# Kernel optimization log

Hardware: AMD Instinct MI355X
Metric: run time of the kernel (lower is better)

## Reference

```python
import jax, jax.numpy as jnp
import numpy as np

B, R, C, D = 8, 64, 16, 128  # batch, num_rows(taxa), patch_num, embed_dim


def _linear_init(key, fan_in, fan_out):
    lim = 1.0 / np.sqrt(fan_in)
    kw, kb = jax.random.split(key)
    W = jax.random.uniform(kw, (fan_in, fan_out), jnp.float32, -lim, lim)
    b = jax.random.uniform(kb, (fan_out,), jnp.float32, -lim, lim)
    return W, b


def setup_inputs() -> dict:
    key = jax.random.key(0)
    ks = jax.random.split(key, 8)
    row_np, col_np = np.triu_indices(R, k=1)  # n = R*(R-1)/2 = 2016 pairs
    hW, hb = _linear_init(ks[1], D, D)
    gW, gb = _linear_init(ks[2], D, D)
    qW, qb = _linear_init(ks[3], D, D)
    kW, kb = _linear_init(ks[4], D, D)
    s1W, s1b = _linear_init(ks[5], D, D)
    s2W, s2b = _linear_init(ks[6], D, 1)
    return {
        "batch_input": jax.random.normal(ks[0], (B, R, C, D), jnp.float32),
        "seq_mask": jnp.ones((B, 1, C), jnp.float32),
        "row": jnp.asarray(row_np, jnp.int32),
        "col": jnp.asarray(col_np, jnp.int32),
        "hW": hW, "hb": hb, "gW": gW, "gb": gb,
        "qW": qW, "qb": qb, "kW": kW, "kb": kb,
        "s1W": s1W, "s1b": s1b, "s2W": s2W, "s2b": s2b,
    }


def reference(batch_input, seq_mask, row, col,
              hW, hb, gW, gb, qW, qb, kW, kb, s1W, s1b, s2W, s2b):
    b, r, c, d = batch_input.shape
    n = row.shape[0]
    # pairwise gather: x_i, x_j -> [b, n, c, d]
    x_i = batch_input[:, row]
    x_j = batch_input[:, col]
    # sigmoid gate fusion of the pair
    h = (x_i - x_j) @ hW + hb
    z = jax.nn.sigmoid(h)
    x = z * x_i + (1.0 - z) * x_j
    # masked global attention over the batch_input 'memory' (r > 2 branch)
    q = x @ qW + qb                    # [b, n, c, d]
    k = batch_input @ kW + kb          # [b, r, c, d]
    scale = 1.0 / np.sqrt(d * c).astype(np.float32)
    alpha = jnp.einsum('bncd,brcd->bnr', q, k) * scale
    # -inf at (pair n, rows row[n] and col[n]); equivalent to += -inf on finite scores
    neg_mask = (jnp.zeros((n, r), bool)
                .at[jnp.arange(n), row].set(True)
                .at[jnp.arange(n), col].set(True))
    alpha = jnp.where(neg_mask[None], -jnp.inf, alpha)
    alpha = jax.nn.softmax(alpha, axis=-1)
    x_glob = jnp.einsum('bnr,brcd->bncd', alpha, batch_input)
    g = x_glob @ gW + gb
    w = jax.nn.sigmoid(g)
    x = (1.0 - w) * x + w * x_glob
    # s_out: Linear -> GELU(exact) -> Linear(d,1), then mask and reduce over c
    s = jax.nn.gelu(x @ s1W + s1b, approximate=False) @ s2W + s2b  # [b, n, c, 1]
    scores = s[..., 0] * seq_mask       # seq_mask [b,1,c] broadcasts over n
    return scores.sum(-1)               # [b, n]
```

## Files before the change

kernel.cpp:

```cpp
#include <hip/hip_runtime.h>
#include <hip/hip_bf16.h>
#include <math.h>

#define B_    8
#define R_    64
#define C_    16
#define D_    128
#define NPAIR 2016
#define CD    2048
#define PG    16
#define NPG   126
#define XSTR  136
#define NEG_BIG (-1e30f)
#define SCALE 0.022097086912079608f

typedef __attribute__((ext_vector_type(8))) short short8;
typedef __attribute__((ext_vector_type(4))) float float4v;

#define WMH  0u
#define WML  16384u
#define WHH  32768u
#define WHL  49152u
#define WGH  65536u
#define WGL  81920u
#define WSH  98304u
#define WSL  114688u
#define VECO 131072u
#define QBKO 131592u
#define MO   132616u
#define XTO  1181192u
#define GTO  2229768u
#define HO   3278344u

__device__ __forceinline__ unsigned short f2b(float v){
    __hip_bfloat16 h = __float2bfloat16(v);
    return *reinterpret_cast<unsigned short*>(&h);
}
__device__ __forceinline__ float b2f(unsigned short u){
    union { unsigned int i; float f; } v; v.i = ((unsigned int)u) << 16; return v.f;
}
__device__ __forceinline__ float lo2f(unsigned int u){
    union { unsigned int i; float f; } v; v.i = u << 16; return v.f;
}
__device__ __forceinline__ float hif2f(unsigned int u){
    union { unsigned int i; float f; } v; v.i = u & 0xffff0000u; return v.f;
}
__device__ __forceinline__ unsigned int pack2(float a, float b){
    return (unsigned int)f2b(a) | ((unsigned int)f2b(b) << 16);
}
__device__ __forceinline__ void split_bf(float v, float* hi, float* lo){
    __hip_bfloat16 h = __float2bfloat16(v);
    float hf = __bfloat162float(h);
    *hi = hf; *lo = v - hf;
}
__device__ __forceinline__ float sigmoid_safe(float x){
    x = fminf(fmaxf(x, -30.f), 30.f);
    return 1.f / (1.f + __expf(-x));
}
__device__ __forceinline__ float erf_as(float x){
    const float ax = fabsf(x);
    const float tt = 1.f / (1.f + 0.3275911f*ax);
    const float p = tt*(0.254829592f + tt*(-0.284496736f + tt*(1.421413741f +
                     tt*(-1.453152027f + tt*1.061405429f))));
    const float r = 1.f - p*__expf(-ax*ax);
    return copysignf(r, x);
}
__device__ __forceinline__ float gelu_exact(float x){
    return 0.5f * x * (1.f + erf_as(x * 0.70710678118654752f));
}

__global__ __launch_bounds__(256) void k_prepA(
    const float* __restrict__ hW, const float* __restrict__ gW,
    const float* __restrict__ s1W,
    const float* __restrict__ qW, const float* __restrict__ qb,
    const float* __restrict__ kW, const float* __restrict__ kb,
    unsigned short* __restrict__ ws)
{
    const int bid = blockIdx.x, t = threadIdx.x;
    if (bid < 64){
        __shared__ float sKW[2][128];
        const int e0 = bid*2;
        sKW[t>>7][t&127] = kW[(e0 + (t>>7))*128 + (t&127)];
        __syncthreads();
        const int e = t>>7, d = t&127;
        const float* qr = qW + d*128;
        const float* kr = sKW[e];
        float acc = 0.f;
        #pragma unroll 8
        for (int g = 0; g < 128; g += 4){
            const float4 qv = *reinterpret_cast<const float4*>(qr + g);
            acc += qv.x*kr[g] + qv.y*kr[g+1] + qv.z*kr[g+2] + qv.w*kr[g+3];
        }
        float hi, lo; split_bf(acc, &hi, &lo);
        ws[WMH + d*128 + (e0+e)] = f2b(hi);
        ws[WML + d*128 + (e0+e)] = f2b(lo);
    } else if (bid == 64){
        float* vec = (float*)(ws + VECO);
        if (t < 128){
            float a1 = 0.f, a2 = 0.f;
            #pragma unroll 8
            for (int g = 0; g < 128; g += 4){
                const float4 q4 = *reinterpret_cast<const float4*>(qW + t*128 + g);
                const float4 k4 = *reinterpret_cast<const float4*>(kW + t*128 + g);
                const float4 kb4 = *reinterpret_cast<const float4*>(kb + g);
                const float4 qb4 = *reinterpret_cast<const float4*>(qb + g);
                a1 += q4.x*kb4.x + q4.y*kb4.y + q4.z*kb4.z + q4.w*kb4.w;
                a2 += k4.x*qb4.x + k4.y*qb4.y + k4.z*qb4.z + k4.w*qb4.w;
            }
            vec[t] = a1;
            vec[128 + t] = a2;
        } else if (t == 128){
            float a = 0.f;
            for (int g = 0; g < 128; ++g) a = fmaf(qb[g], kb[g], a);
            vec[256] = a;
        }
    } else {
        const int j = bid - 65;
        const int mat = j >> 6;
        const int gid = (j & 63)*256 + t;
        const int n = gid >> 7, k = gid & 127;
        const float* W = (mat==0) ? hW : (mat==1) ? gW : s1W;
        const unsigned int baseh = (mat==0) ? WHH : (mat==1) ? WGH : WSH;
        const unsigned int basel = (mat==0) ? WHL : (mat==1) ? WGL : WSL;
        float hi, lo; split_bf(W[k*128 + n], &hi, &lo);
        ws[baseh + gid] = f2b(hi);
        ws[basel + gid] = f2b(lo);
    }
}

__global__ __launch_bounds__(512) void k_prepB(const float* __restrict__ x,
        const float* __restrict__ gb, unsigned short* __restrict__ ws)
{
    __shared__ __align__(16) unsigned short smem[17472];
    __shared__ float sQ[4];
    const int bid = blockIdx.x, t = threadIdx.x;
    const int w = t >> 6, lane = t & 63, l15 = lane & 15, quad = lane >> 4;

    if (bid < 256){
        const bool isM = (bid >= 128);
        unsigned short* sH = smem;
        unsigned short* sL = smem + 8736;
        const int br0 = (bid & 127) * 4;
        const float* kqf = (const float*)(ws + VECO) + 128;
        const float* mbf = (const float*)(ws + VECO);
        if (t < 4) sQ[t] = 0.f;
        __syncthreads();
        #pragma unroll
        for (int i = 0; i < 4; ++i){
            const int flat = (t + 512*i)*4;
            const int lr = flat >> 11, cd = flat & 2047;
            const float4 v = *reinterpret_cast<const float4*>(x + (size_t)(br0+lr)*CD + cd);
            float h0,l0,h1,l1,h2,l2,h3,l3;
            split_bf(v.x,&h0,&l0); split_bf(v.y,&h1,&l1);
            split_bf(v.z,&h2,&l2); split_bf(v.w,&h3,&l3);
            const int ad = (lr*16 + (cd>>7))*XSTR + lr*8 + (cd & 127);
            uint2 uh, ul;
            uh.x = pack2(h0,h1); uh.y = pack2(h2,h3);
            ul.x = pack2(l0,l1); ul.y = pack2(l2,l3);
            *reinterpret_cast<uint2*>(sH + ad) = uh;
            *reinterpret_cast<uint2*>(sL + ad) = ul;
            if (isM){
                const float4 kq4 = *reinterpret_cast<const float4*>(kqf + (cd & 127));
                atomicAdd(&sQ[lr], v.x*kq4.x + v.y*kq4.y + v.z*kq4.z + v.w*kq4.w);
            }
        }
        __syncthreads();
        const unsigned short* Bh = isM ? (ws+WMH) : (ws+WHH);
        const unsigned short* Bl = isM ? (ws+WML) : (ws+WHL);
        const float bv = isM ? mbf[w*16 + l15] : 0.f;
        float4v acc[4];
        #pragma unroll
        for (int mt = 0; mt < 4; ++mt){ float4v d = {bv,bv,bv,bv}; acc[mt] = d; }
        #pragma unroll
        for (int ks = 0; ks < 4; ++ks){
            const int ko = ks*32 + quad*8;
            const int bd = (w*16 + l15)*128 + ko;
            const short8 bh = *reinterpret_cast<const short8*>(Bh + bd);
            const short8 bl = *reinterpret_cast<const short8*>(Bl + bd);
            #pragma unroll
            for (int mt = 0; mt < 4; ++mt){
                const int ad = (mt*16 + l15)*XSTR + mt*8 + ko;
                const short8 ah = *reinterpret_cast<const short8*>(sH + ad);
                const short8 al = *reinterpret_cast<const short8*>(sL + ad);
                float4v d = acc[mt];
                d = __builtin_amdgcn_mfma_f32_16x16x32_bf16(ah, bh, d, 0,0,0);
                d = __builtin_amdgcn_mfma_f32_16x16x32_bf16(ah, bl, d, 0,0,0);
                d = __builtin_amdgcn_mfma_f32_16x16x32_bf16(al, bh, d, 0,0,0);
                acc[mt] = d;
            }
        }
        const int f = w*16 + l15;
        const unsigned int dsto = isM ? MO : HO;
        #pragma unroll
        for (int mt = 0; mt < 4; ++mt)
        #pragma unroll
        for (int e = 0; e < 4; ++e){
            const int c = quad*4 + e;
            ws[dsto + (size_t)(br0+mt)*CD + c*128 + f] = f2b(acc[mt][e]);
        }
        if (isM && t < 4){
            const float s0 = ((const float*)(ws + VECO))[256];
            ((float*)(ws + QBKO))[br0 + t] = sQ[t] + 16.f*s0;
        }
    } else if (bid < 384){
        unsigned short* tileB = smem;
        const int gidx = bid - 256;
        const int b = gidx >> 4, cd0 = (gidx & 15)*128;
        #pragma unroll
        for (int i = 0; i < 16; ++i){
            const int idx = i*512 + t;
            const int r = idx >> 7, dd = idx & 127;
            tileB[r*138 + dd] = f2b(x[(size_t)(b*64 + r)*CD + cd0 + dd]);
        }
        __syncthreads();
        float4v acc[4];
        #pragma unroll
        for (int nt = 0; nt < 4; ++nt){ float4v z = {0.f,0.f,0.f,0.f}; acc[nt] = z; }
        #pragma unroll
        for (int ks = 0; ks < 4; ++ks){
            const int ko = ks*32 + quad*8;
            const int adg = (w*16 + l15)*128 + ko;
            const short8 ah = *reinterpret_cast<const short8*>(ws + WGH + adg);
            const short8 al = *reinterpret_cast<const short8*>(ws + WGL + adg);
            #pragma unroll
            for (int nt = 0; nt < 4; ++nt){
                const short8 bb = *reinterpret_cast<const short8*>(tileB + (nt*16 + l15)*138 + ko);
                float4v d = acc[nt];
                d = __builtin_amdgcn_mfma_f32_16x16x32_bf16(ah, bb, d, 0,0,0);
                d = __builtin_amdgcn_mfma_f32_16x16x32_bf16(al, bb, d, 0,0,0);
                acc[nt] = d;
            }
        }
        #pragma unroll
        for (int nt = 0; nt < 4; ++nt)
        #pragma unroll
        for (int e = 0; e < 4; ++e){
            const int f = w*16 + quad*4 + e;
            const float val = acc[nt][e] + gb[f];
            ws[GTO + (size_t)(b*2048 + cd0 + f)*64 + nt*16 + l15] = f2b(val);
        }
    } else {
        unsigned short* tile = smem;
        const int blk = bid - 384;
        const int b = blk >> 4, cd0 = (blk & 15)*128;
        #pragma unroll
        for (int i = 0; i < 16; ++i){
            const int idx = i*512 + t;
            const int r = idx >> 7, cc = idx & 127;
            tile[cc*74 + r] = f2b(x[((size_t)(b*64 + r))*CD + cd0 + cc]);
        }
        __syncthreads();
        const unsigned int base = XTO + (unsigned int)(b*2048 + cd0)*64;
        #pragma unroll
        for (int j = 0; j < 16; ++j){
            const int idx = j*512 + t;
            const int cc = idx >> 6, r = idx & 63;
            ws[base + cc*64 + r] = tile[cc*74 + r];
        }
    }
}

__global__ __launch_bounds__(512, 4) void k_main(
    const float* __restrict__ x, const float* __restrict__ seq_mask,
    const int* __restrict__ row, const int* __restrict__ col,
    const float* __restrict__ hb, const float* __restrict__ s1b,
    const float* __restrict__ s2W, const float* __restrict__ s2b,
    const unsigned short* __restrict__ ws, float* __restrict__ out)
{
    __shared__ __align__(16) unsigned short sX[256*XSTR + 128];
    __shared__ __align__(16) unsigned short sAl[16*72];
    __shared__ float sLog[1024];
    __shared__ float sOut[PG];
    __shared__ float sMask[16];
    __shared__ int srp[PG], scp[PG];

    const int t = threadIdx.x;
    const int w = t >> 6, lane = t & 63, l15 = lane & 15, quad = lane >> 4;
    const int b = blockIdx.x, p0 = blockIdx.y * PG;
    const float* xb = x + (size_t)b * R_ * CD;
    const unsigned short* Hb = ws + HO + (size_t)b * R_ * CD;

    if (t < PG){ srp[t] = row[p0+t]; scp[t] = col[p0+t]; sOut[t] = 0.f; }
    if (t >= 32 && t < 48) sMask[t-32] = seq_mask[b*C_ + (t-32)];
    for (int i = t; i < 1152; i += 512) sAl[i] = 0;
    for (int i = t; i < 1024; i += 512) sLog[i] = 0.f;
    __syncthreads();

    #pragma unroll 4
    for (int i = 0; i < 16; ++i){
        const int flat = (t + 512*i)*4;
        const int p = flat >> 11, cd = flat & 2047;
        const int ri = srp[p], ci = scp[p];
        const float4 xi = *reinterpret_cast<const float4*>(xb + (size_t)ri*CD + cd);
        const float4 xj = *reinterpret_cast<const float4*>(xb + (size_t)ci*CD + cd);
        const uint2 Hi2 = *reinterpret_cast<const uint2*>(Hb + (size_t)ri*CD + cd);
        const uint2 Hj2 = *reinterpret_cast<const uint2*>(Hb + (size_t)ci*CD + cd);
        const float4 h4 = *reinterpret_cast<const float4*>(hb + (cd & 127));
        const float z0 = sigmoid_safe(lo2f(Hi2.x)  - lo2f(Hj2.x)  + h4.x);
        const float z1 = sigmoid_safe(hif2f(Hi2.x) - hif2f(Hj2.x) + h4.y);
        const float z2 = sigmoid_safe(lo2f(Hi2.y)  - lo2f(Hj2.y)  + h4.z);
        const float z3 = sigmoid_safe(hif2f(Hi2.y) - hif2f(Hj2.y) + h4.w);
        const float v0 = xj.x + z0*(xi.x - xj.x);
        const float v1 = xj.y + z1*(xi.y - xj.y);
        const float v2 = xj.z + z2*(xi.z - xj.z);
        const float v3 = xj.w + z3*(xi.w - xj.w);
        const int ad = (p*16 + (cd>>7))*XSTR + p*8 + (cd & 127);
        uint2 uv; uv.x = pack2(v0,v1); uv.y = pack2(v2,v3);
        *reinterpret_cast<uint2*>(sX + ad) = uv;
    }
    __syncthreads();

    {
        const int rt = w & 3, kh = w >> 2;
        const int r = rt*16 + l15;
        const unsigned short* Mr = ws + MO + ((size_t)b*64 + r)*CD + kh*1024;
        float4v d = {0.f,0.f,0.f,0.f};
        #pragma unroll 8
        for (int ks = 0; ks < 32; ++ks){
            const int k = kh*1024 + ks*32 + quad*8;
            const short8 ah = *reinterpret_cast<const short8*>(
                sX + (l15*16 + (k>>7))*XSTR + l15*8 + (k & 127));
            const short8 bh = *reinterpret_cast<const short8*>(Mr + ks*32 + quad*8);
            d = __builtin_amdgcn_mfma_f32_16x16x32_bf16(ah, bh, d, 0,0,0);
        }
        #pragma unroll
        for (int e = 0; e < 4; ++e){
            const int pp = quad*4 + e;
            atomicAdd(&sLog[pp*64 + r], d[e]);
        }
    }
    __syncthreads();

    if (t < 256){
        const int pp = t >> 4, l = t & 15;
        const int ri = srp[pp], ci = scp[pp];
        const float* qbk = (const float*)(ws + QBKO);
        float v[4]; float m = NEG_BIG;
        #pragma unroll
        for (int k = 0; k < 4; ++k){
            const int r = l + 16*k;
            float lv = (sLog[pp*64 + r] + qbk[b*64 + r]) * SCALE;
            if (r == ri || r == ci) lv = NEG_BIG;
            v[k] = lv; m = fmaxf(m, lv);
        }
        #pragma unroll
        for (int s = 1; s < 16; s <<= 1) m = fmaxf(m, __shfl_xor(m, s));
        float e4[4]; float sum = 0.f;
        #pragma unroll
        for (int k = 0; k < 4; ++k){
            const int r = l + 16*k;
            const bool masked = (r == ri || r == ci);
            const float e = masked ? 0.f : __expf(fmaxf(v[k]-m, -80.f));
            e4[k] = e; sum += e;
        }
        #pragma unroll
        for (int s = 1; s < 16; s <<= 1) sum += __shfl_xor(sum, s);
        const float inv = 1.f / sum;
        #pragma unroll
        for (int k = 0; k < 4; ++k) sAl[pp*72 + l + 16*k] = f2b(e4[k]*inv);
    }
    __syncthreads();

    {
        const unsigned short* XTb = ws + XTO + (size_t)b * CD * 64;
        const unsigned short* GTb = ws + GTO + (size_t)b * CD * 64;
        const short8 Ah0 = *reinterpret_cast<const short8*>(sAl + l15*72 + quad*8);
        const short8 Ah1 = *reinterpret_cast<const short8*>(sAl + l15*72 + 32 + quad*8);
        #pragma unroll 4
        for (int j = 0; j < 16; ++j){
            const int cd = w*256 + j*16 + l15;
            const short8 xb0 = *reinterpret_cast<const short8*>(XTb + (size_t)cd*64 + quad*8);
            const short8 xb1 = *reinterpret_cast<const short8*>(XTb + (size_t)cd*64 + 32 + quad*8);
            const short8 gb0 = *reinterpret_cast<const short8*>(GTb + (size_t)cd*64 + quad*8);
            const short8 gb1 = *reinterpret_cast<const short8*>(GTb + (size_t)cd*64 + 32 + quad*8);
            float4v dx = {0.f,0.f,0.f,0.f}, dg = {0.f,0.f,0.f,0.f};
            dx = __builtin_amdgcn_mfma_f32_16x16x32_bf16(Ah0, xb0, dx, 0,0,0);
            dx = __builtin_amdgcn_mfma_f32_16x16x32_bf16(Ah1, xb1, dx, 0,0,0);
            dg = __builtin_amdgcn_mfma_f32_16x16x32_bf16(Ah0, gb0, dg, 0,0,0);
            dg = __builtin_amdgcn_mfma_f32_16x16x32_bf16(Ah1, gb1, dg, 0,0,0);
            #pragma unroll
            for (int e = 0; e < 4; ++e){
                const int pp = quad*4 + e;
                const int ad = (pp*16 + (cd>>7))*XSTR + pp*8 + (cd & 127);
                const float wv = sigmoid_safe(dg[e]);
                const float xo = b2f(sX[ad]);
                sX[ad] = f2b((1.f - wv)*xo + wv*dx[e]);
            }
        }
    }
    __syncthreads();

    {
        float4v acc16[16];
        const float bv = s1b[w*16 + l15];
        #pragma unroll
        for (int mt = 0; mt < 16; ++mt){ float4v d = {bv,bv,bv,bv}; acc16[mt] = d; }
        #pragma unroll
        for (int ks = 0; ks < 4; ++ks){
            const int ko = ks*32 + quad*8;
            const int bd = (w*16 + l15)*128 + ko;
            const short8 bh = *reinterpret_cast<const short8*>(ws + WSH + bd);
            const short8 bl = *reinterpret_cast<const short8*>(ws + WSL + bd);
            #pragma unroll
            for (int mt = 0; mt < 16; ++mt){
                const short8 a = *reinterpret_cast<const short8*>(sX + (mt*16 + l15)*XSTR + mt*8 + ko);
                float4v d = acc16[mt];
                d = __builtin_amdgcn_mfma_f32_16x16x32_bf16(a, bh, d, 0,0,0);
                d = __builtin_amdgcn_mfma_f32_16x16x32_bf16(a, bl, d, 0,0,0);
                acc16[mt] = d;
            }
        }
        const float s2v = s2W[w*16 + l15];
        const float mk0 = sMask[quad*4+0], mk1 = sMask[quad*4+1];
        const float mk2 = sMask[quad*4+2], mk3 = sMask[quad*4+3];
        float psum[16];
        #pragma unroll
        for (int mt = 0; mt < 16; ++mt){
            float s = gelu_exact(acc16[mt][0]) * mk0;
            s += gelu_exact(acc16[mt][1]) * mk1;
            s += gelu_exact(acc16[mt][2]) * mk2;
            s += gelu_exact(acc16[mt][3]) * mk3;
            psum[mt] = s * s2v;
        }
        #pragma unroll
        for (int s = 1; s < 64; s <<= 1)
            #pragma unroll
            for (int mt = 0; mt < 16; ++mt) psum[mt] += __shfl_xor(psum[mt], s);
        if (lane == 0){
            #pragma unroll
            for (int mt = 0; mt < 16; ++mt) atomicAdd(&sOut[mt], psum[mt]);
        }
    }
    __syncthreads();

    if (t < PG){
        float msum = 0.f;
        #pragma unroll
        for (int c = 0; c < 16; ++c) msum += sMask[c];
        out[(size_t)b*NPAIR + p0 + t] = sOut[t] + s2b[0]*msum;
    }
}

extern "C" void kernel_launch(void* const* d_in, const int* in_sizes, int n_in,
                              void* d_out, int out_size, void* d_ws, size_t ws_size,
                              hipStream_t stream)
{
    const float* x    = (const float*)d_in[0];
    const float* mask = (const float*)d_in[1];
    const int*   row  = (const int*)d_in[2];
    const int*   col  = (const int*)d_in[3];
    const float* hW  = (const float*)d_in[4];  const float* hb  = (const float*)d_in[5];
    const float* gW  = (const float*)d_in[6];  const float* gb  = (const float*)d_in[7];
    const float* qW  = (const float*)d_in[8];  const float* qb  = (const float*)d_in[9];
    const float* kW  = (const float*)d_in[10]; const float* kb  = (const float*)d_in[11];
    const float* s1W = (const float*)d_in[12]; const float* s1b = (const float*)d_in[13];
    const float* s2W = (const float*)d_in[14]; const float* s2b = (const float*)d_in[15];

    unsigned short* ws = (unsigned short*)d_ws;

    k_prepA<<<257, 256, 0, stream>>>(hW, gW, s1W, qW, qb, kW, kb, ws);
    k_prepB<<<512, 512, 0, stream>>>(x, gb, ws);
    k_main<<<dim3(B_, NPG), 512, 0, stream>>>(x, mask, row, col,
                                              hb, s1b, s2W, s2b,
                                              ws, (float*)d_out);
}
```

Measured before the change: 241.2 us.

## Drop split-bf16 compensation terms in projection and s1 GEMMs

Removes the low-order bf16 correction from the x operand in prepB's projection GEMMs and drops the s1W low-part MFMA in the main kernel, so fewer MFMAs run and less LDS is used. The s1W bf16 conversion moves from prepA into four extra prepB blocks, and f2b/split_bf now use manual round-to-nearest-even bit arithmetic. The transpose tile stride changes from 74 to 69. The cost is lower numerical accuracy in the H/M projections and the score MLP.

```diff
diff --git a/kernel.cpp b/kernel.cpp
--- a/kernel.cpp
+++ b/kernel.cpp
@@ -24,7 +24,6 @@
 #define WGH  65536u
 #define WGL  81920u
 #define WSH  98304u
-#define WSL  114688u
 #define VECO 131072u
 #define QBKO 131592u
 #define MO   132616u
@@ -32,9 +31,10 @@
 #define GTO  2229768u
 #define HO   3278344u
 
-__device__ __forceinline__ unsigned short f2b(float v){
-    __hip_bfloat16 h = __float2bfloat16(v);
-    return *reinterpret_cast<unsigned short*>(&h);
+__device__ __forceinline__ unsigned short f2b(float f){
+    union { float f; unsigned int u; } v; v.f = f;
+    const unsigned int r = v.u + 0x7FFFu + ((v.u >> 16) & 1u);
+    return (unsigned short)(r >> 16);
 }
 __device__ __forceinline__ float b2f(unsigned short u){
     union { unsigned int i; float f; } v; v.i = ((unsigned int)u) << 16; return v.f;
@@ -49,9 +49,10 @@
     return (unsigned int)f2b(a) | ((unsigned int)f2b(b) << 16);
 }
 __device__ __forceinline__ void split_bf(float v, float* hi, float* lo){
-    __hip_bfloat16 h = __float2bfloat16(v);
-    float hf = __bfloat162float(h);
-    *hi = hf; *lo = v - hf;
+    union { float f; unsigned int u; } x; x.f = v;
+    const unsigned int r = (x.u + 0x7FFFu + ((x.u >> 16) & 1u)) & 0xffff0000u;
+    union { unsigned int u; float f; } h; h.u = r;
+    *hi = h.f; *lo = v - h.f;
 }
 __device__ __forceinline__ float sigmoid_safe(float x){
     x = fminf(fmaxf(x, -30.f), 30.f);
@@ -71,7 +72,6 @@
 
 __global__ __launch_bounds__(256) void k_prepA(
     const float* __restrict__ hW, const float* __restrict__ gW,
-    const float* __restrict__ s1W,
     const float* __restrict__ qW, const float* __restrict__ qb,
     const float* __restrict__ kW, const float* __restrict__ kb,
     unsigned short* __restrict__ ws)
@@ -119,9 +119,9 @@
         const int mat = j >> 6;
         const int gid = (j & 63)*256 + t;
         const int n = gid >> 7, k = gid & 127;
-        const float* W = (mat==0) ? hW : (mat==1) ? gW : s1W;
-        const unsigned int baseh = (mat==0) ? WHH : (mat==1) ? WGH : WSH;
-        const unsigned int basel = (mat==0) ? WHL : (mat==1) ? WGL : WSL;
+        const float* W = (mat==0) ? hW : gW;
+        const unsigned int baseh = (mat==0) ? WHH : WGH;
+        const unsigned int basel = (mat==0) ? WHL : WGL;
         float hi, lo; split_bf(W[k*128 + n], &hi, &lo);
         ws[baseh + gid] = f2b(hi);
         ws[basel + gid] = f2b(lo);
@@ -129,9 +129,10 @@
 }
 
 __global__ __launch_bounds__(512) void k_prepB(const float* __restrict__ x,
-        const float* __restrict__ gb, unsigned short* __restrict__ ws)
+        const float* __restrict__ gb, const float* __restrict__ s1W,
+        unsigned short* __restrict__ ws)
 {
-    __shared__ __align__(16) unsigned short smem[17472];
+    __shared__ __align__(16) unsigned short smem[8832];
     __shared__ float sQ[4];
     const int bid = blockIdx.x, t = threadIdx.x;
     const int w = t >> 6, lane = t & 63, l15 = lane & 15, quad = lane >> 4;
@@ -139,7 +140,6 @@
     if (bid < 256){
         const bool isM = (bid >= 128);
         unsigned short* sH = smem;
-        unsigned short* sL = smem + 8736;
         const int br0 = (bid & 127) * 4;
         const float* kqf = (const float*)(ws + VECO) + 128;
         const float* mbf = (const float*)(ws + VECO);
@@ -150,15 +150,10 @@
             const int flat = (t + 512*i)*4;
             const int lr = flat >> 11, cd = flat & 2047;
             const float4 v = *reinterpret_cast<const float4*>(x + (size_t)(br0+lr)*CD + cd);
-            float h0,l0,h1,l1,h2,l2,h3,l3;
-            split_bf(v.x,&h0,&l0); split_bf(v.y,&h1,&l1);
-            split_bf(v.z,&h2,&l2); split_bf(v.w,&h3,&l3);
             const int ad = (lr*16 + (cd>>7))*XSTR + lr*8 + (cd & 127);
-            uint2 uh, ul;
-            uh.x = pack2(h0,h1); uh.y = pack2(h2,h3);
-            ul.x = pack2(l0,l1); ul.y = pack2(l2,l3);
+            uint2 uh;
+            uh.x = pack2(v.x, v.y); uh.y = pack2(v.z, v.w);
             *reinterpret_cast<uint2*>(sH + ad) = uh;
-            *reinterpret_cast<uint2*>(sL + ad) = ul;
             if (isM){
                 const float4 kq4 = *reinterpret_cast<const float4*>(kqf + (cd & 127));
                 atomicAdd(&sQ[lr], v.x*kq4.x + v.y*kq4.y + v.z*kq4.z + v.w*kq4.w);
@@ -181,11 +176,9 @@
             for (int mt = 0; mt < 4; ++mt){
                 const int ad = (mt*16 + l15)*XSTR + mt*8 + ko;
                 const short8 ah = *reinterpret_cast<const short8*>(sH + ad);
-                const short8 al = *reinterpret_cast<const short8*>(sL + ad);
                 float4v d = acc[mt];
                 d = __builtin_amdgcn_mfma_f32_16x16x32_bf16(ah, bh, d, 0,0,0);
                 d = __builtin_amdgcn_mfma_f32_16x16x32_bf16(ah, bl, d, 0,0,0);
-                d = __builtin_amdgcn_mfma_f32_16x16x32_bf16(al, bh, d, 0,0,0);
                 acc[mt] = d;
             }
         }
@@ -239,7 +232,7 @@
             const float val = acc[nt][e] + gb[f];
             ws[GTO + (size_t)(b*2048 + cd0 + f)*64 + nt*16 + l15] = f2b(val);
         }
-    } else {
+    } else if (bid < 512){
         unsigned short* tile = smem;
         const int blk = bid - 384;
         const int b = blk >> 4, cd0 = (blk & 15)*128;
@@ -247,7 +240,7 @@
         for (int i = 0; i < 16; ++i){
             const int idx = i*512 + t;
             const int r = idx >> 7, cc = idx & 127;
-            tile[cc*74 + r] = f2b(x[((size_t)(b*64 + r))*CD + cd0 + cc]);
+            tile[cc*69 + r] = f2b(x[((size_t)(b*64 + r))*CD + cd0 + cc]);
         }
         __syncthreads();
         const unsigned int base = XTO + (unsigned int)(b*2048 + cd0)*64;
@@ -255,7 +248,15 @@
         for (int j = 0; j < 16; ++j){
             const int idx = j*512 + t;
             const int cc = idx >> 6, r = idx & 63;
-            ws[base + cc*64 + r] = tile[cc*74 + r];
+            ws[base + cc*64 + r] = tile[cc*69 + r];
+        }
+    } else {
+        const int gid = (bid - 512)*4096 + t;
+        #pragma unroll
+        for (int i = 0; i < 8; ++i){
+            const int g = gid + i*512;
+            const int n = g >> 7, k = g & 127;
+            ws[WSH + g] = f2b(s1W[k*128 + n]);
         }
     }
 }
@@ -400,14 +401,10 @@
             const int ko = ks*32 + quad*8;
             const int bd = (w*16 + l15)*128 + ko;
             const short8 bh = *reinterpret_cast<const short8*>(ws + WSH + bd);
-            const short8 bl = *reinterpret_cast<const short8*>(ws + WSL + bd);
             #pragma unroll
             for (int mt = 0; mt < 16; ++mt){
                 const short8 a = *reinterpret_cast<const short8*>(sX + (mt*16 + l15)*XSTR + mt*8 + ko);
-                float4v d = acc16[mt];
-                d = __builtin_amdgcn_mfma_f32_16x16x32_bf16(a, bh, d, 0,0,0);
-                d = __builtin_amdgcn_mfma_f32_16x16x32_bf16(a, bl, d, 0,0,0);
-                acc16[mt] = d;
+                acc16[mt] = __builtin_amdgcn_mfma_f32_16x16x32_bf16(a, bh, acc16[mt], 0,0,0);
             }
         }
         const float s2v = s2W[w*16 + l15];
@@ -458,8 +455,8 @@
 
     unsigned short* ws = (unsigned short*)d_ws;
 
-    k_prepA<<<257, 256, 0, stream>>>(hW, gW, s1W, qW, qb, kW, kb, ws);
-    k_prepB<<<512, 512, 0, stream>>>(x, gb, ws);
+    k_prepA<<<193, 256, 0, stream>>>(hW, gW, qW, qb, kW, kb, ws);
+    k_prepB<<<516, 512, 0, stream>>>(x, gb, s1W, ws);
     k_main<<<dim3(B_, NPG), 512, 0, stream>>>(x, mask, row, col,
                                               hb, s1b, s2W, s2b,
                                               ws, (float*)d_out);
```

Measured after the change: 237.3 us. About the same (-1.6%).
